# Performance work log

Hardware: AMD Instinct MI355X
Metric: run time of the kernel (lower is better)

Reference implementation:

```python
import jax, jax.numpy as jnp
import numpy as np

WS = 8        # window_size
NH = 8        # num_heads
SHIFT = WS // 2  # cyclic shift amount (shift=True)
EPS = 1e-5


def _layernorm(x, g, b):
    m = x.mean(-1, keepdims=True)
    v = ((x - m) ** 2).mean(-1, keepdims=True)
    return (x - m) * jax.lax.rsqrt(v + EPS) * g + b


def setup_inputs() -> dict:
    key = jax.random.key(0)
    ks = jax.random.split(key, 6)
    B, C, H, W = 8, 256, 128, 128
    hidden = 4 * C
    return {
        "x": jax.random.normal(ks[0], (B, C, H, W), dtype=jnp.float32),
        "norm1_g": jnp.ones((C,), jnp.float32),
        "norm1_b": jnp.zeros((C,), jnp.float32),
        "w_qkv": 0.02 * jax.random.normal(ks[1], (C, 3 * C), dtype=jnp.float32),
        "b_qkv": jnp.zeros((3 * C,), jnp.float32),
        "w_proj": 0.02 * jax.random.normal(ks[2], (C, C), dtype=jnp.float32),
        "b_proj": jnp.zeros((C,), jnp.float32),
        "norm2_g": jnp.ones((C,), jnp.float32),
        "norm2_b": jnp.zeros((C,), jnp.float32),
        "w1": 0.02 * jax.random.normal(ks[3], (C, hidden), dtype=jnp.float32),
        "b1": jnp.zeros((hidden,), jnp.float32),
        "w2": 0.02 * jax.random.normal(ks[4], (hidden, C), dtype=jnp.float32),
        "b2": jnp.zeros((C,), jnp.float32),
    }


def reference(x, norm1_g, norm1_b, w_qkv, b_qkv, w_proj, b_proj,
              norm2_g, norm2_b, w1, b1, w2, b2):
    B, C, H, W = x.shape
    hd = C // NH
    scale = hd ** -0.5

    xh = jnp.transpose(x, (0, 2, 3, 1))          # B,H,W,C
    shortcut = xh
    y = _layernorm(xh, norm1_g, norm1_b)
    y = jnp.roll(y, (-SHIFT, -SHIFT), axis=(1, 2))  # cyclic shift

    # window partition -> (Bw, N, C), N = WS*WS
    y = y.reshape(B, H // WS, WS, W // WS, WS, C)
    y = y.transpose(0, 1, 3, 2, 4, 5).reshape(-1, WS * WS, C)
    Bw, N, _ = y.shape

    qkv = (y @ w_qkv + b_qkv).reshape(Bw, N, 3, NH, hd).transpose(2, 0, 3, 1, 4)
    q, k, v = qkv[0], qkv[1], qkv[2]             # each (Bw, NH, N, hd)
    att = jax.nn.softmax(jnp.einsum('bhnd,bhmd->bhnm', q, k) * scale, axis=-1)
    o = jnp.einsum('bhnm,bhmd->bhnd', att, v)
    o = o.transpose(0, 2, 1, 3).reshape(Bw, N, C) @ w_proj + b_proj

    # window reverse -> B,H,W,C
    y = o.reshape(B, H // WS, W // WS, WS, WS, C)
    y = y.transpose(0, 1, 3, 2, 4, 5).reshape(B, H, W, C)
    y = jnp.roll(y, (SHIFT, SHIFT), axis=(1, 2))  # reverse shift

    xh = y + shortcut                             # attention residual

    # MLP branch: computed in the original module but its output is DISCARDED
    # (original returns `x + shortcut` where shortcut == x, i.e. 2*x).
    h = _layernorm(xh, norm2_g, norm2_b)
    h = jax.nn.gelu(h @ w1 + b1, approximate=False) @ w2 + b2  # unused, faithful to source

    out = xh + xh                                 # replicates original `x + shortcut`
    return jnp.transpose(out, (0, 3, 1, 2))       # back to B,C,H,W
```

## Files before the change

kernel.cpp:

```cpp
#include <hip/hip_runtime.h>
#include <stdint.h>

#define SHIFT 4
#define EPS 1e-5f

#define B_ 8
#define C_ 256
#define H_ 128
#define W_ 128
#define HW_ (H_*W_)
#define NWIN 2048

typedef unsigned short u16;
typedef float f32x4 __attribute__((ext_vector_type(4)));
typedef __bf16 bf16x8 __attribute__((ext_vector_type(8)));
typedef unsigned short u16x8 __attribute__((ext_vector_type(8)));
typedef unsigned short u16x4 __attribute__((ext_vector_type(4)));

static __device__ __forceinline__ u16 f2bf(float f) {
    uint32_t u = __builtin_bit_cast(uint32_t, f);
    u = u + 0x7fffu + ((u >> 16) & 1u);
    return (u16)(u >> 16);
}
static __device__ __forceinline__ float bf2f(u16 u) {
    return __builtin_bit_cast(float, (uint32_t)u << 16);
}

__global__ __launch_bounds__(256) void k_prep_w(const float* __restrict__ wqkv,
                                                const float* __restrict__ wproj,
                                                u16* __restrict__ W2q, u16* __restrict__ W2pA) {
    int i = blockIdx.x * 256 + threadIdx.x;
    if (i < 48 * 8 * 64 * 8) {
        int e = i & 7, l = (i >> 3) & 63, kt = (i >> 9) & 7, jg = i >> 12;
        int col = jg * 16 + (l & 15);
        int k = kt * 32 + (l >> 4) * 8 + e;
        W2q[i] = f2bf(wqkv[k * 768 + col]);
    } else {
        int j = i - 48 * 8 * 64 * 8;
        int e = j & 7, l = (j >> 3) & 63, kt = (j >> 9) & 7, ig = j >> 12;
        int c = ig * 16 + (l & 15);
        int k = kt * 32 + (l >> 4) * 8 + e;
        W2pA[j] = f2bf(wproj[k * 256 + c]);
    }
}

__global__ __launch_bounds__(256) void k_ln_win(const float* __restrict__ x,
                                                const float* __restrict__ g,
                                                const float* __restrict__ beta,
                                                u16* __restrict__ ywin2) {
    __shared__ u16 sv[256][130];
    __shared__ float ps[2][128];
    __shared__ float pss[2][128];
    __shared__ float mval[128];
    __shared__ float rval[128];
    int h = blockIdx.x;
    int b = blockIdx.y;
    int t = threadIdx.x;
    int p = t >> 7, w = t & 127;
    const float* xb = x + (size_t)b * C_ * HW_ + (size_t)h * W_;
    float s = 0.f, ss = 0.f;
    #pragma unroll 8
    for (int it = 0; it < 128; ++it) {
        int c = it * 2 + p;
        float v = xb[(size_t)c * HW_ + w];
        s += v; ss += v * v;
        sv[c][w] = f2bf(v);
    }
    ps[p][w] = s;
    pss[p][w] = ss;
    __syncthreads();
    if (t < 128) {
        float st = ps[0][t] + ps[1][t];
        float sst = pss[0][t] + pss[1][t];
        float m = st * (1.f / C_);
        float var = sst * (1.f / C_) - m * m;
        mval[t] = m;
        rval[t] = rsqrtf(var + EPS);
    }
    __syncthreads();
    int hp = (h - SHIFT) & 127;
    int wh = hp >> 3, r = hp & 7;
    int i_f = r >> 1;
    int lrb = (r & 1) * 8;
    int c = t;
    float gc = g[c], bc = beta[c];
    int kt = c >> 5, lk2 = (c >> 3) & 3, e = c & 7;
    int winrow = (b * 16 + wh) * 16;
    u16* dst = ywin2 + (size_t)winrow * 16384 + kt * 2048 + i_f * 512 + lk2 * 128 + lrb * 8 + e;
    #pragma unroll 4
    for (int wp = 0; wp < 128; ++wp) {
        int wsrc = (wp + SHIFT) & 127;
        float v = bf2f(sv[c][wsrc]);
        float yv = (v - mval[wsrc]) * rval[wsrc] * gc + bc;
        dst[(size_t)(wp >> 3) * 16384 + (wp & 7) * 8] = f2bf(yv);
    }
}

__global__ __launch_bounds__(512, 4) void k_fused(const u16* __restrict__ ywin2,
                                                  const u16* __restrict__ W2q,
                                                  const u16* __restrict__ W2pA,
                                                  const float* __restrict__ bqkv,
                                                  const float* __restrict__ bproj,
                                                  const float* __restrict__ x,
                                                  float* __restrict__ out) {
    extern __shared__ __align__(16) char smem[];
    int bid = blockIdx.x;
    int win = (bid & 7) * 256 + (bid >> 3);
    int b = win >> 8, wh = (win >> 4) & 15, ww = win & 15;
    int t = threadIdx.x;
    int wave = t >> 6, lane = t & 63;
    int lr = lane & 15, lk = lane >> 4;
    int hd = wave;

    u16* WR = (u16*)smem + wave * 5120;
    u16* Q  = WR;
    u16* K  = WR + 2560;
    u16* VT = WR;
    u16* Ph = WR + 2560;
    u16* O  = (u16*)smem;

    const u16* afp = ywin2 + (size_t)win * 16384;

    f32x4 acc[4][4];
    #pragma unroll
    for (int i = 0; i < 4; ++i)
        #pragma unroll
        for (int j = 0; j < 4; ++j) acc[i][j] = (f32x4){0.f,0.f,0.f,0.f};
    #pragma unroll 2
    for (int kt = 0; kt < 8; ++kt) {
        bf16x8 af[4], bq[4];
        #pragma unroll
        for (int i = 0; i < 4; ++i)
            af[i] = __builtin_bit_cast(bf16x8, *(const u16x8*)(afp + kt * 2048 + i * 512 + lane * 8));
        #pragma unroll
        for (int jl = 0; jl < 4; ++jl) {
            int jg = (jl >> 1) * 16 + 2 * hd + (jl & 1);
            bq[jl] = __builtin_bit_cast(bf16x8, *(const u16x8*)(W2q + ((size_t)(jg * 8 + kt)) * 512 + lane * 8));
        }
        #pragma unroll
        for (int i = 0; i < 4; ++i)
            #pragma unroll
            for (int jl = 0; jl < 4; ++jl)
                acc[i][jl] = __builtin_amdgcn_mfma_f32_16x16x32_bf16(af[i], bq[jl], acc[i][jl], 0, 0, 0);
    }
    #pragma unroll
    for (int jl = 0; jl < 4; ++jl) {
        int which = jl >> 1;
        int d = (jl & 1) * 16 + lr;
        float bi = bqkv[which * 256 + hd * 32 + d];
        u16* dst = which ? K : Q;
        #pragma unroll
        for (int i = 0; i < 4; ++i)
            #pragma unroll
            for (int rg = 0; rg < 4; ++rg)
                dst[(i * 16 + lk * 4 + rg) * 40 + d] = f2bf(acc[i][jl][rg] + bi);
    }
    bf16x8 qf[4], kf[4];
    #pragma unroll
    for (int i = 0; i < 4; ++i)
        qf[i] = __builtin_bit_cast(bf16x8, *(const u16x8*)(&Q[(i * 16 + lr) * 40 + lk * 8]));
    #pragma unroll
    for (int j = 0; j < 4; ++j)
        kf[j] = __builtin_bit_cast(bf16x8, *(const u16x8*)(&K[(j * 16 + lr) * 40 + lk * 8]));
    f32x4 s[4][4];
    #pragma unroll
    for (int i = 0; i < 4; ++i)
        #pragma unroll
        for (int j = 0; j < 4; ++j) s[i][j] = (f32x4){0.f,0.f,0.f,0.f};
    #pragma unroll
    for (int i = 0; i < 4; ++i)
        #pragma unroll
        for (int j = 0; j < 4; ++j)
            s[i][j] = __builtin_amdgcn_mfma_f32_16x16x32_bf16(qf[i], kf[j], s[i][j], 0, 0, 0);

    const float scale = 0.17677669529663687f;
    #pragma unroll
    for (int i = 0; i < 4; ++i) {
        #pragma unroll
        for (int rg = 0; rg < 4; ++rg) {
            float s0 = s[i][0][rg] * scale, s1 = s[i][1][rg] * scale;
            float s2 = s[i][2][rg] * scale, s3 = s[i][3][rg] * scale;
            float mx = fmaxf(fmaxf(s0, s1), fmaxf(s2, s3));
            mx = fmaxf(mx, __shfl_xor(mx, 1));
            mx = fmaxf(mx, __shfl_xor(mx, 2));
            mx = fmaxf(mx, __shfl_xor(mx, 4));
            mx = fmaxf(mx, __shfl_xor(mx, 8));
            float p0 = __expf(s0 - mx), p1 = __expf(s1 - mx);
            float p2 = __expf(s2 - mx), p3 = __expf(s3 - mx);
            float sm = p0 + p1 + p2 + p3;
            sm += __shfl_xor(sm, 1);
            sm += __shfl_xor(sm, 2);
            sm += __shfl_xor(sm, 4);
            sm += __shfl_xor(sm, 8);
            float rs = 1.f / sm;
            s[i][0][rg] = p0 * rs; s[i][1][rg] = p1 * rs;
            s[i][2][rg] = p2 * rs; s[i][3][rg] = p3 * rs;
        }
    }
    #pragma unroll
    for (int j2 = 0; j2 < 2; ++j2)
        #pragma unroll
        for (int i = 0; i < 4; ++i)
            #pragma unroll
            for (int rg = 0; rg < 4; ++rg)
                Ph[(i * 16 + lk * 4 + rg) * 40 + j2 * 16 + lr] = f2bf(s[i][j2][rg]);

    f32x4 av[4][2];
    #pragma unroll
    for (int i = 0; i < 4; ++i)
        #pragma unroll
        for (int j = 0; j < 2; ++j) av[i][j] = (f32x4){0.f,0.f,0.f,0.f};
    #pragma unroll 2
    for (int kt = 0; kt < 8; ++kt) {
        bf16x8 af[4], bv[2];
        #pragma unroll
        for (int i = 0; i < 4; ++i)
            af[i] = __builtin_bit_cast(bf16x8, *(const u16x8*)(afp + kt * 2048 + i * 512 + lane * 8));
        #pragma unroll
        for (int jl = 0; jl < 2; ++jl) {
            int jg = 32 + 2 * hd + jl;
            bv[jl] = __builtin_bit_cast(bf16x8, *(const u16x8*)(W2q + ((size_t)(jg * 8 + kt)) * 512 + lane * 8));
        }
        #pragma unroll
        for (int i = 0; i < 4; ++i)
            #pragma unroll
            for (int jl = 0; jl < 2; ++jl)
                av[i][jl] = __builtin_amdgcn_mfma_f32_16x16x32_bf16(af[i], bv[jl], av[i][jl], 0, 0, 0);
    }
    #pragma unroll
    for (int jl = 0; jl < 2; ++jl) {
        float bi = bqkv[512 + hd * 32 + jl * 16 + lr];
        #pragma unroll
        for (int i = 0; i < 4; ++i) {
            u16x4 pk;
            #pragma unroll
            for (int rg = 0; rg < 4; ++rg) pk[rg] = f2bf(av[i][jl][rg] + bi);
            *(u16x4*)(&VT[(jl * 16 + lr) * 72 + i * 16 + lk * 4]) = pk;
        }
    }
    f32x4 oacc[4][2];
    #pragma unroll
    for (int i = 0; i < 4; ++i)
        #pragma unroll
        for (int j = 0; j < 2; ++j) oacc[i][j] = (f32x4){0.f,0.f,0.f,0.f};
    {
        bf16x8 pf[4], vf[2];
        #pragma unroll
        for (int i = 0; i < 4; ++i)
            pf[i] = __builtin_bit_cast(bf16x8, *(const u16x8*)(&Ph[(i * 16 + lr) * 40 + lk * 8]));
        #pragma unroll
        for (int j = 0; j < 2; ++j)
            vf[j] = __builtin_bit_cast(bf16x8, *(const u16x8*)(&VT[(j * 16 + lr) * 72 + lk * 8]));
        #pragma unroll
        for (int i = 0; i < 4; ++i)
            #pragma unroll
            for (int j = 0; j < 2; ++j)
                oacc[i][j] = __builtin_amdgcn_mfma_f32_16x16x32_bf16(pf[i], vf[j], oacc[i][j], 0, 0, 0);
    }
    #pragma unroll
    for (int j2 = 2; j2 < 4; ++j2)
        #pragma unroll
        for (int i = 0; i < 4; ++i)
            #pragma unroll
            for (int rg = 0; rg < 4; ++rg)
                Ph[(i * 16 + lk * 4 + rg) * 40 + (j2 & 1) * 16 + lr] = f2bf(s[i][j2][rg]);
    {
        bf16x8 pf[4], vf[2];
        #pragma unroll
        for (int i = 0; i < 4; ++i)
            pf[i] = __builtin_bit_cast(bf16x8, *(const u16x8*)(&Ph[(i * 16 + lr) * 40 + lk * 8]));
        #pragma unroll
        for (int j = 0; j < 2; ++j)
            vf[j] = __builtin_bit_cast(bf16x8, *(const u16x8*)(&VT[(j * 16 + lr) * 72 + 32 + lk * 8]));
        #pragma unroll
        for (int i = 0; i < 4; ++i)
            #pragma unroll
            for (int j = 0; j < 2; ++j)
                oacc[i][j] = __builtin_amdgcn_mfma_f32_16x16x32_bf16(pf[i], vf[j], oacc[i][j], 0, 0, 0);
    }

    __syncthreads();
    #pragma unroll
    for (int i = 0; i < 4; ++i)
        #pragma unroll
        for (int j = 0; j < 2; ++j)
            #pragma unroll
            for (int rg = 0; rg < 4; ++rg)
                O[(i * 16 + lk * 4 + rg) * 280 + hd * 32 + j * 16 + lr] = f2bf(oacc[i][j][rg]);
    __syncthreads();

    f32x4 c2[2][4];
    #pragma unroll
    for (int i = 0; i < 2; ++i)
        #pragma unroll
        for (int j = 0; j < 4; ++j) c2[i][j] = (f32x4){0.f,0.f,0.f,0.f};
    #pragma unroll 2
    for (int kt = 0; kt < 8; ++kt) {
        bf16x8 a2[2], bo[4];
        #pragma unroll
        for (int i2 = 0; i2 < 2; ++i2)
            a2[i2] = __builtin_bit_cast(bf16x8,
                *(const u16x8*)(W2pA + ((size_t)((wave * 2 + i2) * 8 + kt)) * 512 + lane * 8));
        #pragma unroll
        for (int j = 0; j < 4; ++j)
            bo[j] = __builtin_bit_cast(bf16x8, *(const u16x8*)(&O[(j * 16 + lr) * 280 + kt * 32 + lk * 8]));
        #pragma unroll
        for (int i2 = 0; i2 < 2; ++i2)
            #pragma unroll
            for (int j = 0; j < 4; ++j)
                c2[i2][j] = __builtin_amdgcn_mfma_f32_16x16x32_bf16(a2[i2], bo[j], c2[i2][j], 0, 0, 0);
    }

    {
        int hbase = wh * 8 + SHIFT;
        int wbase = ww * 8 + SHIFT;
        #pragma unroll
        for (int i = 0; i < 2; ++i)
            #pragma unroll
            for (int rg = 0; rg < 4; ++rg) {
                int c = wave * 32 + i * 16 + lk * 4 + rg;
                float bi = bproj[c];
                size_t cb = ((size_t)(b * 256 + c)) << 14;
                #pragma unroll
                for (int j = 0; j < 4; ++j) {
                    int token = j * 16 + lr;
                    int r = token >> 3, sgm = token & 7;
                    int hs = (hbase + r) & 127;
                    int wc = (wbase + sgm) & 127;
                    size_t oi = cb + hs * 128 + wc;
                    out[oi] = 2.f * (c2[i][j][rg] + bi + x[oi]);
                }
            }
    }
}

extern "C" void kernel_launch(void* const* d_in, const int* in_sizes, int n_in,
                              void* d_out, int out_size, void* d_ws, size_t ws_size,
                              hipStream_t stream) {
    const float* x     = (const float*)d_in[0];
    const float* g1    = (const float*)d_in[1];
    const float* bb1   = (const float*)d_in[2];
    const float* wqkv  = (const float*)d_in[3];
    const float* bqkv  = (const float*)d_in[4];
    const float* wproj = (const float*)d_in[5];
    const float* bproj = (const float*)d_in[6];
    float* out = (float*)d_out;

    char* ws = (char*)d_ws;
    u16* W2q  = (u16*)ws;
    u16* W2pA = (u16*)(ws + 393216);
    u16* ywin2 = (u16*)(ws + (1ull << 20));

    static const int LDS_BYTES = 81920;
    hipFuncSetAttribute((const void*)k_fused,
                        hipFuncAttributeMaxDynamicSharedMemorySize, LDS_BYTES);

    k_prep_w<<<1024, 256, 0, stream>>>(wqkv, wproj, W2q, W2pA);
    k_ln_win<<<dim3(128, 8), 256, 0, stream>>>(x, g1, bb1, ywin2);
    k_fused<<<NWIN, 512, LDS_BYTES, stream>>>(ywin2, W2q, W2pA, bqkv, bproj, x, out);
}
```

Baseline: 243.8 us.

## Fuse LayerNorm and window partition into the fused attention kernel

Removes the separate LayerNorm/shift/window-partition kernel. Each fused block now reads its own 64 shifted pixels across all 256 channels from x, computes the statistics with wave shuffles, and writes normalized bf16 values to a per-window global buffer that it reads back after a barrier. This saves a kernel launch and the separate pass over x, but the reads stride across channels with poor coalescing (8 consecutive floats per 64-lane wave). x is also read twice per block, and the block relies on __syncthreads for global-memory visibility of its own writes.

```diff
diff --git a/kernel.cpp b/kernel.cpp
--- a/kernel.cpp
+++ b/kernel.cpp
@@ -44,64 +44,15 @@
     }
 }
 
-__global__ __launch_bounds__(256) void k_ln_win(const float* __restrict__ x,
-                                                const float* __restrict__ g,
-                                                const float* __restrict__ beta,
-                                                u16* __restrict__ ywin2) {
-    __shared__ u16 sv[256][130];
-    __shared__ float ps[2][128];
-    __shared__ float pss[2][128];
-    __shared__ float mval[128];
-    __shared__ float rval[128];
-    int h = blockIdx.x;
-    int b = blockIdx.y;
-    int t = threadIdx.x;
-    int p = t >> 7, w = t & 127;
-    const float* xb = x + (size_t)b * C_ * HW_ + (size_t)h * W_;
-    float s = 0.f, ss = 0.f;
-    #pragma unroll 8
-    for (int it = 0; it < 128; ++it) {
-        int c = it * 2 + p;
-        float v = xb[(size_t)c * HW_ + w];
-        s += v; ss += v * v;
-        sv[c][w] = f2bf(v);
-    }
-    ps[p][w] = s;
-    pss[p][w] = ss;
-    __syncthreads();
-    if (t < 128) {
-        float st = ps[0][t] + ps[1][t];
-        float sst = pss[0][t] + pss[1][t];
-        float m = st * (1.f / C_);
-        float var = sst * (1.f / C_) - m * m;
-        mval[t] = m;
-        rval[t] = rsqrtf(var + EPS);
-    }
-    __syncthreads();
-    int hp = (h - SHIFT) & 127;
-    int wh = hp >> 3, r = hp & 7;
-    int i_f = r >> 1;
-    int lrb = (r & 1) * 8;
-    int c = t;
-    float gc = g[c], bc = beta[c];
-    int kt = c >> 5, lk2 = (c >> 3) & 3, e = c & 7;
-    int winrow = (b * 16 + wh) * 16;
-    u16* dst = ywin2 + (size_t)winrow * 16384 + kt * 2048 + i_f * 512 + lk2 * 128 + lrb * 8 + e;
-    #pragma unroll 4
-    for (int wp = 0; wp < 128; ++wp) {
-        int wsrc = (wp + SHIFT) & 127;
-        float v = bf2f(sv[c][wsrc]);
-        float yv = (v - mval[wsrc]) * rval[wsrc] * gc + bc;
-        dst[(size_t)(wp >> 3) * 16384 + (wp & 7) * 8] = f2bf(yv);
-    }
-}
-
-__global__ __launch_bounds__(512, 4) void k_fused(const u16* __restrict__ ywin2,
+
+__global__ __launch_bounds__(512, 4) void k_fused(u16* __restrict__ ywin2,
                                                   const u16* __restrict__ W2q,
                                                   const u16* __restrict__ W2pA,
                                                   const float* __restrict__ bqkv,
                                                   const float* __restrict__ bproj,
                                                   const float* __restrict__ x,
+                                                  const float* __restrict__ g1,
+                                                  const float* __restrict__ bb1,
                                                   float* __restrict__ out) {
     extern __shared__ __align__(16) char smem[];
     int bid = blockIdx.x;
@@ -118,6 +69,38 @@
     u16* VT = WR;
     u16* Ph = WR + 2560;
     u16* O  = (u16*)smem;
+
+    {
+        int r_t = wave;
+        int s_t = lane & 7;
+        int cgrp = lane >> 3;
+        int hs = (wh * 8 + r_t + SHIFT) & 127;
+        int ws = (ww * 8 + s_t + SHIFT) & 127;
+        const float* xrow = x + (((size_t)b * C_) << 14) + hs * W_ + ws;
+        float sa = 0.f, sb = 0.f;
+        #pragma unroll 8
+        for (int cc = 0; cc < 32; ++cc) {
+            int c = cc * 8 + cgrp;
+            float v = xrow[(size_t)c * HW_];
+            sa += v; sb += v * v;
+        }
+        sa += __shfl_xor(sa, 8);  sb += __shfl_xor(sb, 8);
+        sa += __shfl_xor(sa, 16); sb += __shfl_xor(sb, 16);
+        sa += __shfl_xor(sa, 32); sb += __shfl_xor(sb, 32);
+        float m = sa * (1.f / 256.f);
+        float var = sb * (1.f / 256.f) - m * m;
+        float rv = rsqrtf(var + EPS);
+        u16* ydst = ywin2 + (size_t)win * 16384
+                  + (r_t >> 1) * 512 + ((r_t & 1) * 8 + s_t) * 8 + cgrp;
+        #pragma unroll 8
+        for (int cc = 0; cc < 32; ++cc) {
+            int c = cc * 8 + cgrp;
+            float v = xrow[(size_t)c * HW_];
+            float yv = (v - m) * rv * g1[c] + bb1[c];
+            ydst[(cc >> 2) * 2048 + (cc & 3) * 128] = f2bf(yv);
+        }
+    }
+    __syncthreads();
 
     const u16* afp = ywin2 + (size_t)win * 16384;
 
@@ -356,6 +339,5 @@
                         hipFuncAttributeMaxDynamicSharedMemorySize, LDS_BYTES);
 
     k_prep_w<<<1024, 256, 0, stream>>>(wqkv, wproj, W2q, W2pA);
-    k_ln_win<<<dim3(128, 8), 256, 0, stream>>>(x, g1, bb1, ywin2);
-    k_fused<<<NWIN, 512, LDS_BYTES, stream>>>(ywin2, W2q, W2pA, bqkv, bproj, x, out);
-}
+    k_fused<<<NWIN, 512, LDS_BYTES, stream>>>(ywin2, W2q, W2pA, bqkv, bproj, x, g1, bb1, out);
+}
```

Result: slower. 314.9 us (+29.2%).
